# Kernel optimization log

Measured on AMD Instinct MI355X. Metric: run time of the kernel, lower is better.

The kernel has to match this reference:

```python
import jax, jax.numpy as jnp
import numpy as np

N_NODES = 50000
N_EDGES = 800000
NEG_SLOPE = 0.2  # PyG GATConv default


def _gat_layer(x, src, dst, n, W, a_src, a_dst, b, concat):
    """One GATConv layer (PyG semantics, eval mode so attention dropout is off).

    x: [N, F_in], src/dst: [E'] (self loops included), W: [F_in, H*C],
    a_src/a_dst: [H, C], b: [H*C] if concat else [C].
    """
    H, C = a_src.shape
    h = (x @ W).reshape(n, H, C)                      # [N, H, C]
    al_s = jnp.sum(h * a_src, axis=-1)                # [N, H]
    al_d = jnp.sum(h * a_dst, axis=-1)                # [N, H]
    e = jax.nn.leaky_relu(al_s[src] + al_d[dst], NEG_SLOPE)  # [E', H]
    # numerically stable softmax over incoming edges of each dst node
    m = jax.lax.stop_gradient(jax.ops.segment_max(e, dst, num_segments=n))
    m = jnp.where(jnp.isfinite(m), m, 0.0)
    ex = jnp.exp(e - m[dst])                          # [E', H]
    denom = jax.ops.segment_sum(ex, dst, num_segments=n)     # [N, H]
    alpha = ex / denom[dst]                           # safe: self loops => denom > 0
    out = jax.ops.segment_sum(alpha[:, :, None] * h[src], dst, num_segments=n)  # [N,H,C]
    out = out.reshape(n, H * C) if concat else out.mean(axis=1)
    return out + b


def setup_inputs() -> dict:
    key = jax.random.key(0)
    ks = jax.random.split(key, 8)
    in_dim, hid, heads, out_dim = 256, 32, 8, 16
    x = jax.random.normal(ks[0], (N_NODES, in_dim), dtype=jnp.float32)
    edge_index = jax.random.randint(ks[1], (2, N_EDGES), 0, N_NODES, dtype=jnp.int64)
    s1 = 1.0 / np.sqrt(in_dim)
    s2 = 1.0 / np.sqrt(heads * hid)
    return {
        "x": x,
        "edge_index": edge_index,
        "W1": jax.random.normal(ks[2], (in_dim, heads * hid), dtype=jnp.float32) * s1,
        "a_src1": jax.random.normal(ks[3], (heads, hid), dtype=jnp.float32) * s2,
        "a_dst1": jax.random.normal(ks[4], (heads, hid), dtype=jnp.float32) * s2,
        "b1": jnp.zeros((heads * hid,), dtype=jnp.float32),
        "W2": jax.random.normal(ks[5], (heads * hid, out_dim), dtype=jnp.float32) * s2,
        "a_src2": jax.random.normal(ks[6], (1, out_dim), dtype=jnp.float32) * 0.25,
        "a_dst2": jax.random.normal(ks[7], (1, out_dim), dtype=jnp.float32) * 0.25,
        "b2": jnp.zeros((out_dim,), dtype=jnp.float32),
    }


def reference(x, edge_index, W1, a_src1, a_dst1, b1, W2, a_src2, a_dst2, b2):
    n = x.shape[0]
    loops = jnp.arange(n, dtype=edge_index.dtype)
    src = jnp.concatenate([edge_index[0], loops])  # add_self_loops (PyG default)
    dst = jnp.concatenate([edge_index[1], loops])
    h = jax.nn.relu(_gat_layer(x, src, dst, n, W1, a_src1, a_dst1, b1, concat=True))
    # F.dropout(p=0.5, training=False) -> identity in eval mode
    h = _gat_layer(h, src, dst, n, W2, a_src2, a_dst2, b2, concat=False)
    return jax.nn.log_softmax(h, axis=1)
```

## Files before the change

### kernel.cpp

```cpp
#include <hip/hip_runtime.h>
#include <hip/hip_bf16.h>


#define LRELU(x) ((x) > 0.f ? (x) : 0.2f * (x))

typedef __attribute__((ext_vector_type(8))) short short8;
typedef __attribute__((ext_vector_type(8))) unsigned short ushort8;
typedef __attribute__((ext_vector_type(4))) float f32x4;

__device__ inline unsigned short f2b(float f) {
    __hip_bfloat16 h = __float2bfloat16(f);
    return *reinterpret_cast<unsigned short*>(&h);
}
__device__ inline float b2f(unsigned short u) {
    __hip_bfloat16 h;
    *reinterpret_cast<unsigned short*>(&h) = u;
    return __bfloat162float(h);
}


__global__ __launch_bounds__(256) void k_prep(const int* __restrict__ dst, int* deg, int E,
                                              const float* __restrict__ W1,
                                              unsigned short* __restrict__ W1t,
                                              const float* __restrict__ W2,
                                              unsigned short* __restrict__ W2t,
                                              const float* __restrict__ x,
                                              unsigned short* __restrict__ xb,
                                              int NX, int HB) {
    int b = blockIdx.x, t = threadIdx.x;
    if (b < HB) {
        int i = b * 256 + t;
        if (i < E) atomicAdd(&deg[dst[i]], 1);
    } else if (b < HB + 256) {
        int k = b - HB;
        W1t[t * 256 + k] = f2b(W1[k * 256 + t]);
    } else if (b < HB + 256 + 16) {
        int nn = b - HB - 256;
        W2t[nn * 256 + t] = f2b(W2[t * 16 + nn]);
    } else {
        int i = ((b - HB - 272) * 256 + t) * 8;
        if (i < NX) {
            const float4* sp = (const float4*)(x + i);
            float4 f0 = sp[0], f1 = sp[1];
            ushort8 o;
            o[0] = f2b(f0.x); o[1] = f2b(f0.y); o[2] = f2b(f0.z); o[3] = f2b(f0.w);
            o[4] = f2b(f1.x); o[5] = f2b(f1.y); o[6] = f2b(f1.z); o[7] = f2b(f1.w);
            *(ushort8*)(xb + i) = o;
        }
    }
}


__global__ __launch_bounds__(256) void k_scanA(const int* __restrict__ deg,
                                               int* __restrict__ tmp,
                                               int* __restrict__ blocksum, int n) {
    __shared__ int sc[256];
    int b = blockIdx.x, t = threadIdx.x;
    int i = b * 256 + t;
    int v = (i < n) ? deg[i] + 1 : 0;
    sc[t] = v;
    __syncthreads();
    for (int off = 1; off < 256; off <<= 1) {
        int x = 0;
        if (t >= off) x = sc[t - off];
        __syncthreads();
        sc[t] += x;
        __syncthreads();
    }
    if (i < n) tmp[i] = sc[t] - v;
    if (t == 255) blocksum[b] = sc[255];
}


__global__ __launch_bounds__(256) void k_scanC(const int* __restrict__ tmp,
                                               const int* __restrict__ blocksum,
                                               int* __restrict__ offs,
                                               int* __restrict__ cursor,
                                               int n, int P, int nb) {
    __shared__ int sc[256];
    __shared__ int base;
    int b = blockIdx.x, t = threadIdx.x;
    int v = (t < nb) ? blocksum[t] : 0;
    sc[t] = v;
    __syncthreads();
    for (int off = 1; off < 256; off <<= 1) {
        int x = 0;
        if (t >= off) x = sc[t - off];
        __syncthreads();
        sc[t] += x;
        __syncthreads();
    }
    if (t == 0) base = (b == 0) ? 0 : sc[b - 1];
    __syncthreads();
    int i = b * 256 + t;
    if (i < n) {
        int o = tmp[i] + base;
        offs[i] = o;
        cursor[i] = o;
    }
    if (b == 0 && t == 0) offs[n] = P;
}


__global__ __launch_bounds__(256) void k_g1sc(const unsigned short* __restrict__ Ab,
                                              const unsigned short* __restrict__ Wt,
                                              unsigned short* __restrict__ h1b,
                                              const float* __restrict__ asrc,
                                              const float* __restrict__ adst,
                                              float* __restrict__ als,
                                              float* __restrict__ ald, int M, int GB,
                                              const int* __restrict__ src,
                                              const int* __restrict__ dstv,
                                              int* cursor, int* __restrict__ csr, int E) {
    __shared__ unsigned short As[128][40];
    __shared__ unsigned short Bs[128][40];
    int t = threadIdx.x;
    int b = blockIdx.x;
    if (b >= GB) {
        int i = (b - GB) * 256 + t;
        int s, d;
        if (i < E) {
            s = src[i];
            d = dstv[i];
        } else if (i < E + M) {
            s = i - E;
            d = s;
        } else {
            return;
        }
        int p = atomicAdd(&cursor[d], 1);
        csr[p] = s;
        return;
    }
    int r0 = (b >> 1) * 128, c0 = (b & 1) * 128;
    int srow = t >> 1, shalf = t & 1;
    int lane = t & 63, w = t >> 6;
    int lane15 = lane & 15, quad = lane >> 4;
    int rbw = (w & 1) * 64, cbw = (w >> 1) * 64;

    f32x4 acc[4][4];
#pragma unroll
    for (int i = 0; i < 4; i++)
#pragma unroll
        for (int j = 0; j < 4; j++) acc[i][j] = (f32x4)0.f;

    for (int k0 = 0; k0 < 256; k0 += 32) {
        {
            int row = r0 + srow;
            ushort8 p0, p1;
            if (row < M) {
                const ushort8* ap = (const ushort8*)&Ab[(size_t)row * 256 + k0 + shalf * 16];
                p0 = ap[0];
                p1 = ap[1];
            } else {
                p0 = (ushort8)0; p1 = (ushort8)0;
            }
            *(ushort8*)&As[srow][shalf * 16] = p0;
            *(ushort8*)&As[srow][shalf * 16 + 8] = p1;
            const ushort8* bp = (const ushort8*)&Wt[(size_t)(c0 + srow) * 256 + k0 + shalf * 16];
            *(ushort8*)&Bs[srow][shalf * 16] = bp[0];
            *(ushort8*)&Bs[srow][shalf * 16 + 8] = bp[1];
        }
        __syncthreads();
        short8 af[4], bf[4];
#pragma unroll
        for (int i = 0; i < 4; i++)
            af[i] = *(const short8*)&As[rbw + i * 16 + lane15][quad * 8];
#pragma unroll
        for (int j = 0; j < 4; j++)
            bf[j] = *(const short8*)&Bs[cbw + j * 16 + lane15][quad * 8];
#pragma unroll
        for (int i = 0; i < 4; i++)
#pragma unroll
            for (int j = 0; j < 4; j++)
                acc[i][j] = __builtin_amdgcn_mfma_f32_16x16x32_bf16(af[i], bf[j], acc[i][j], 0, 0, 0);
        __syncthreads();
    }

    float asv[4], adv[4];
#pragma unroll
    for (int j = 0; j < 4; j++) {
        asv[j] = asrc[c0 + cbw + j * 16 + lane15];
        adv[j] = adst[c0 + cbw + j * 16 + lane15];
    }
    int hb = (c0 + cbw) >> 5;
#pragma unroll
    for (int i = 0; i < 4; i++) {
        int rowb = r0 + rbw + i * 16 + quad * 4;
#pragma unroll
        for (int j = 0; j < 4; j++) {
            int col = c0 + cbw + j * 16 + lane15;
#pragma unroll
            for (int r = 0; r < 4; r++) {
                int row = rowb + r;
                if (row < M) h1b[(size_t)row * 256 + col] = f2b(acc[i][j][r]);
            }
        }
#pragma unroll
        for (int m = 0; m < 2; m++) {
#pragma unroll
            for (int r = 0; r < 4; r++) {
                float ps = acc[i][2 * m][r] * asv[2 * m] + acc[i][2 * m + 1][r] * asv[2 * m + 1];
                float pd = acc[i][2 * m][r] * adv[2 * m] + acc[i][2 * m + 1][r] * adv[2 * m + 1];
#pragma unroll
                for (int off = 1; off < 16; off <<= 1) {
                    ps += __shfl_xor(ps, off, 16);
                    pd += __shfl_xor(pd, off, 16);
                }
                int row = rowb + r;
                if (lane15 == 0 && row < M) {
                    als[(size_t)row * 8 + hb + m] = ps;
                    ald[(size_t)row * 8 + hb + m] = pd;
                }
            }
        }
    }
}


__global__ __launch_bounds__(128) void k_agg1(const int* __restrict__ csr,
                                              const int* __restrict__ offs,
                                              const float* __restrict__ als,
                                              const float* __restrict__ aldg,
                                              const unsigned short* __restrict__ h1b,
                                              const float* __restrict__ b1,
                                              unsigned short* __restrict__ x2b) {
    int v = blockIdx.x;
    int t = threadIdx.x;
    int start = offs[v];
    int deg = offs[v + 1] - start;
    __shared__ float aldv[8];
    __shared__ int su[32];
    __shared__ float ws[8 * 33];
    if (t < 8) aldv[t] = aldg[v * 8 + t];
    __syncthreads();
    int h = t >> 4;
    const unsigned int* __restrict__ hbase = (const unsigned int*)h1b;
    float a0 = 0.f, a1 = 0.f, wsum = 0.f;
    for (int base = 0; base < deg; base += 32) {
        int cnt = min(32, deg - base);
        int cnt4 = (cnt + 3) & ~3;
        if (base) __syncthreads();
        if (t < cnt4) {
            if (t < cnt) {
                int u = csr[start + base + t];
                su[t] = u;
                const float4* ap = (const float4*)(als + (size_t)u * 8);
                float4 x0 = ap[0], x1 = ap[1];
                ws[0 * 33 + t] = __expf(LRELU(x0.x + aldv[0]));
                ws[1 * 33 + t] = __expf(LRELU(x0.y + aldv[1]));
                ws[2 * 33 + t] = __expf(LRELU(x0.z + aldv[2]));
                ws[3 * 33 + t] = __expf(LRELU(x0.w + aldv[3]));
                ws[4 * 33 + t] = __expf(LRELU(x1.x + aldv[4]));
                ws[5 * 33 + t] = __expf(LRELU(x1.y + aldv[5]));
                ws[6 * 33 + t] = __expf(LRELU(x1.z + aldv[6]));
                ws[7 * 33 + t] = __expf(LRELU(x1.w + aldv[7]));
            } else {
                su[t] = v;
#pragma unroll
                for (int k = 0; k < 8; k++) ws[k * 33 + t] = 0.f;
            }
        }
        __syncthreads();
        for (int e = 0; e < cnt4; e += 4) {
            int u0 = su[e + 0], u1 = su[e + 1], u2 = su[e + 2], u3 = su[e + 3];
            float w0 = ws[h * 33 + e + 0];
            float w1 = ws[h * 33 + e + 1];
            float w2 = ws[h * 33 + e + 2];
            float w3 = ws[h * 33 + e + 3];
            unsigned int pk0 = hbase[u0 * 128 + t];
            unsigned int pk1 = hbase[u1 * 128 + t];
            unsigned int pk2 = hbase[u2 * 128 + t];
            unsigned int pk3 = hbase[u3 * 128 + t];
            a0 += w0 * __uint_as_float(pk0 << 16);
            a1 += w0 * __uint_as_float(pk0 & 0xffff0000u);
            a0 += w1 * __uint_as_float(pk1 << 16);
            a1 += w1 * __uint_as_float(pk1 & 0xffff0000u);
            a0 += w2 * __uint_as_float(pk2 << 16);
            a1 += w2 * __uint_as_float(pk2 & 0xffff0000u);
            a0 += w3 * __uint_as_float(pk3 << 16);
            a1 += w3 * __uint_as_float(pk3 & 0xffff0000u);
            wsum += (w0 + w1) + (w2 + w3);
        }
    }
    const float2* b1v = (const float2*)b1;
    float2 bb = b1v[t];
    float inv = 1.0f / wsum;
    float o0 = a0 * inv + bb.x;
    float o1 = a1 * inv + bb.y;
    o0 = o0 > 0.f ? o0 : 0.f;
    o1 = o1 > 0.f ? o1 : 0.f;
    unsigned int opk = (unsigned int)f2b(o0) | ((unsigned int)f2b(o1) << 16);
    ((unsigned int*)(x2b + (size_t)v * 256))[t] = opk;
}


__global__ __launch_bounds__(256) void k_gemm2(const unsigned short* __restrict__ Xb,
                                               const unsigned short* __restrict__ W2t,
                                               const float* __restrict__ asrc,
                                               const float* __restrict__ adst,
                                               unsigned short* __restrict__ h2b,
                                               float* __restrict__ als,
                                               float* __restrict__ ald, int n) {
    int t = threadIdx.x;
    int lane = t & 63, w = t >> 6;
    int lane15 = lane & 15, quad = lane >> 4;
    int row0 = blockIdx.x * 64 + w * 16;
    f32x4 acc = (f32x4)0.f;
#pragma unroll
    for (int k0 = 0; k0 < 256; k0 += 32) {
        short8 a = *(const short8*)&Xb[(size_t)(row0 + lane15) * 256 + k0 + quad * 8];
        short8 b = *(const short8*)&W2t[lane15 * 256 + k0 + quad * 8];
        acc = __builtin_amdgcn_mfma_f32_16x16x32_bf16(a, b, acc, 0, 0, 0);
    }
    float asv = asrc[lane15], adv = adst[lane15];
#pragma unroll
    for (int r = 0; r < 4; r++) {
        int row = row0 + quad * 4 + r;
        float hv = acc[r];
        float ps = hv * asv, pd = hv * adv;
#pragma unroll
        for (int off = 1; off < 16; off <<= 1) {
            ps += __shfl_xor(ps, off, 16);
            pd += __shfl_xor(pd, off, 16);
        }
        if (row < n) {
            h2b[(size_t)row * 16 + lane15] = f2b(hv);
            if (lane15 == 0) {
                als[row] = ps;
                ald[row] = pd;
            }
        }
    }
}


__global__ __launch_bounds__(256) void k_agg2(const int* __restrict__ csr,
                                              const int* __restrict__ offs,
                                              const float* __restrict__ als,
                                              const float* __restrict__ aldg,
                                              const unsigned short* __restrict__ h2b,
                                              const float* __restrict__ b2,
                                              float* __restrict__ out, int n) {
    int v = blockIdx.x * 4 + (threadIdx.x >> 6);
    if (v >= n) return;
    int lane = threadIdx.x & 63;
    int start = offs[v];
    int deg = offs[v + 1] - start;
    float aldv = aldg[v];
    int c = lane & 15, q = lane >> 4;
    float acc = 0.f, wsum = 0.f;
    for (int e = q; e < deg; e += 4) {
        int u = csr[start + e];
        float x = als[u] + aldv;
        float wv = __expf(LRELU(x));
        acc += wv * b2f(h2b[(size_t)u * 16 + c]);
        wsum += wv;
    }
    acc += __shfl_xor(acc, 32, 64);
    acc += __shfl_xor(acc, 16, 64);
    wsum += __shfl_xor(wsum, 32, 64);
    wsum += __shfl_xor(wsum, 16, 64);
    float o = acc / wsum + b2[c];
    float mx = o;
#pragma unroll
    for (int off = 8; off; off >>= 1) mx = fmaxf(mx, __shfl_xor(mx, off, 16));
    float s = __expf(o - mx);
#pragma unroll
    for (int off = 8; off; off >>= 1) s += __shfl_xor(s, off, 16);
    float res = o - mx - __logf(s);
    if (q == 0) out[(size_t)v * 16 + c] = res;
}


extern "C" void kernel_launch(void* const* d_in, const int* in_sizes, int n_in,
                              void* d_out, int out_size, void* d_ws, size_t ws_size,
                              hipStream_t stream) {
    const float* x = (const float*)d_in[0];
    const int* ei = (const int*)d_in[1];
    const float* W1 = (const float*)d_in[2];
    const float* asrc1 = (const float*)d_in[3];
    const float* adst1 = (const float*)d_in[4];
    const float* b1 = (const float*)d_in[5];
    const float* W2 = (const float*)d_in[6];
    const float* asrc2 = (const float*)d_in[7];
    const float* adst2 = (const float*)d_in[8];
    const float* b2 = (const float*)d_in[9];
    float* out = (float*)d_out;

    int n = in_sizes[0] / 256;
    int E = in_sizes[1] / 2;
    int P = E + n;
    const int* src = ei;
    const int* dst = ei + E;
    int NB = (n + 255) / 256;
    int HB = (E + 255) / 256;
    int NX = n * 256;
    int XB = (NX + 2047) / 2048;
    int GB = ((n + 127) / 128) * 2;
    int SB = (P + 255) / 256;

    char* p = (char*)d_ws;
    auto alloc = [&](size_t bytes) {
        void* r = (void*)p;
        p += (bytes + 255) & ~(size_t)255;
        return r;
    };
    unsigned short* h1b = (unsigned short*)alloc((size_t)n * 256 * 2);
    unsigned short* x2b = (unsigned short*)alloc((size_t)n * 256 * 2);
    unsigned short* xb = (unsigned short*)alloc((size_t)n * 256 * 2);
    unsigned short* W1t = (unsigned short*)alloc((size_t)256 * 256 * 2);
    unsigned short* W2t = (unsigned short*)alloc((size_t)16 * 256 * 2);
    float* als1 = (float*)alloc((size_t)n * 8 * 4);
    float* ald1 = (float*)alloc((size_t)n * 8 * 4);
    unsigned short* h2b = (unsigned short*)alloc((size_t)n * 16 * 2);
    float* als2 = (float*)alloc((size_t)n * 4);
    float* ald2 = (float*)alloc((size_t)n * 4);
    int* deg = (int*)alloc((size_t)n * 4);
    int* offs = (int*)alloc((size_t)(n + 1) * 4);
    int* cursor = (int*)alloc((size_t)n * 4);
    int* stmp = (int*)alloc((size_t)n * 4);
    int* blocksum = (int*)alloc((size_t)NB * 4);
    int* csr = (int*)alloc((size_t)P * 4);

    hipMemsetAsync(deg, 0, (size_t)n * 4, stream);
    k_prep<<<HB + 272 + XB, 256, 0, stream>>>(dst, deg, E, W1, W1t, W2, W2t, x, xb, NX, HB);
    k_scanA<<<NB, 256, 0, stream>>>(deg, stmp, blocksum, n);
    k_scanC<<<NB, 256, 0, stream>>>(stmp, blocksum, offs, cursor, n, P, NB);

    k_g1sc<<<GB + SB, 256, 0, stream>>>(xb, W1t, h1b, asrc1, adst1, als1, ald1, n, GB,
                                        src, dst, cursor, csr, E);
    k_agg1<<<n, 128, 0, stream>>>(csr, offs, als1, ald1, h1b, b1, x2b);

    k_gemm2<<<(n + 63) / 64, 256, 0, stream>>>(x2b, W2t, asrc2, adst2, h2b, als2, ald2, n);
    k_agg2<<<(n + 3) / 4, 256, 0, stream>>>(csr, offs, als2, ald2, h2b, b2, out, n);
}
```

Measured before the change: 341.2 us.

## Merge CSR build and weight/input conversion into one cooperative kernel

```diff
diff --git a/kernel.cpp b/kernel.cpp
--- a/kernel.cpp
+++ b/kernel.cpp
@@ -1,6 +1,9 @@
 #include <hip/hip_runtime.h>
 #include <hip/hip_bf16.h>
-
+#include <hip/hip_cooperative_groups.h>
+
+
+namespace cg = cooperative_groups;
 
 #define LRELU(x) ((x) > 0.f ? (x) : 0.2f * (x))
 
@@ -19,120 +22,112 @@
 }
 
 
-__global__ __launch_bounds__(256) void k_prep(const int* __restrict__ dst, int* deg, int E,
-                                              const float* __restrict__ W1,
-                                              unsigned short* __restrict__ W1t,
-                                              const float* __restrict__ W2,
-                                              unsigned short* __restrict__ W2t,
-                                              const float* __restrict__ x,
-                                              unsigned short* __restrict__ xb,
-                                              int NX, int HB) {
-    int b = blockIdx.x, t = threadIdx.x;
-    if (b < HB) {
-        int i = b * 256 + t;
-        if (i < E) atomicAdd(&deg[dst[i]], 1);
-    } else if (b < HB + 256) {
-        int k = b - HB;
-        W1t[t * 256 + k] = f2b(W1[k * 256 + t]);
-    } else if (b < HB + 256 + 16) {
-        int nn = b - HB - 256;
-        W2t[nn * 256 + t] = f2b(W2[t * 16 + nn]);
-    } else {
-        int i = ((b - HB - 272) * 256 + t) * 8;
-        if (i < NX) {
-            const float4* sp = (const float4*)(x + i);
-            float4 f0 = sp[0], f1 = sp[1];
-            ushort8 o;
-            o[0] = f2b(f0.x); o[1] = f2b(f0.y); o[2] = f2b(f0.z); o[3] = f2b(f0.w);
-            o[4] = f2b(f1.x); o[5] = f2b(f1.y); o[6] = f2b(f1.z); o[7] = f2b(f1.w);
-            *(ushort8*)(xb + i) = o;
-        }
-    }
-}
-
-
-__global__ __launch_bounds__(256) void k_scanA(const int* __restrict__ deg,
-                                               int* __restrict__ tmp,
-                                               int* __restrict__ blocksum, int n) {
-    __shared__ int sc[256];
-    int b = blockIdx.x, t = threadIdx.x;
-    int i = b * 256 + t;
-    int v = (i < n) ? deg[i] + 1 : 0;
-    sc[t] = v;
-    __syncthreads();
-    for (int off = 1; off < 256; off <<= 1) {
-        int x = 0;
-        if (t >= off) x = sc[t - off];
-        __syncthreads();
-        sc[t] += x;
-        __syncthreads();
-    }
-    if (i < n) tmp[i] = sc[t] - v;
-    if (t == 255) blocksum[b] = sc[255];
-}
-
-
-__global__ __launch_bounds__(256) void k_scanC(const int* __restrict__ tmp,
-                                               const int* __restrict__ blocksum,
-                                               int* __restrict__ offs,
-                                               int* __restrict__ cursor,
-                                               int n, int P, int nb) {
+__global__ __launch_bounds__(256) void k_csr(const int* __restrict__ src,
+                                             const int* __restrict__ dst,
+                                             int* deg, int* tmp, int* blocksum,
+                                             int* offs, int* cursor, int* __restrict__ csr,
+                                             const float* __restrict__ W1,
+                                             unsigned short* __restrict__ W1t,
+                                             const float* __restrict__ W2,
+                                             unsigned short* __restrict__ W2t,
+                                             const float* __restrict__ x,
+                                             unsigned short* __restrict__ xb,
+                                             int n, int E, int P, int NB, int NX) {
+    cg::grid_group grid = cg::this_grid();
     __shared__ int sc[256];
     __shared__ int base;
     int b = blockIdx.x, t = threadIdx.x;
-    int v = (t < nb) ? blocksum[t] : 0;
-    sc[t] = v;
-    __syncthreads();
-    for (int off = 1; off < 256; off <<= 1) {
-        int x = 0;
-        if (t >= off) x = sc[t - off];
-        __syncthreads();
-        sc[t] += x;
-        __syncthreads();
-    }
-    if (t == 0) base = (b == 0) ? 0 : sc[b - 1];
-    __syncthreads();
-    int i = b * 256 + t;
-    if (i < n) {
-        int o = tmp[i] + base;
-        offs[i] = o;
-        cursor[i] = o;
-    }
-    if (b == 0 && t == 0) offs[n] = P;
-}
-
-
-__global__ __launch_bounds__(256) void k_g1sc(const unsigned short* __restrict__ Ab,
-                                              const unsigned short* __restrict__ Wt,
-                                              unsigned short* __restrict__ h1b,
-                                              const float* __restrict__ asrc,
-                                              const float* __restrict__ adst,
-                                              float* __restrict__ als,
-                                              float* __restrict__ ald, int M, int GB,
-                                              const int* __restrict__ src,
-                                              const int* __restrict__ dstv,
-                                              int* cursor, int* __restrict__ csr, int E) {
+    int gid = b * 256 + t;
+    int gsz = gridDim.x * 256;
+
+    for (int i = gid; i < n; i += gsz) deg[i] = 0;
+    for (int i = gid; i < 65536; i += gsz) {
+        int k = i >> 8, nn = i & 255;
+        W1t[nn * 256 + k] = f2b(W1[k * 256 + nn]);
+    }
+    for (int i = gid; i < 4096; i += gsz) {
+        int nn = i >> 8, k = i & 255;
+        W2t[nn * 256 + k] = f2b(W2[k * 16 + nn]);
+    }
+    for (int i = gid * 8; i < NX; i += gsz * 8) {
+        const float4* sp = (const float4*)(x + i);
+        float4 f0 = sp[0], f1 = sp[1];
+        ushort8 o;
+        o[0] = f2b(f0.x); o[1] = f2b(f0.y); o[2] = f2b(f0.z); o[3] = f2b(f0.w);
+        o[4] = f2b(f1.x); o[5] = f2b(f1.y); o[6] = f2b(f1.z); o[7] = f2b(f1.w);
+        *(ushort8*)(xb + i) = o;
+    }
+    grid.sync();
+
+    for (int i = gid; i < E; i += gsz) atomicAdd(&deg[dst[i]], 1);
+    grid.sync();
+
+    if (b < NB) {
+        int i = b * 256 + t;
+        int v = (i < n) ? deg[i] + 1 : 0;
+        sc[t] = v;
+        __syncthreads();
+        for (int off = 1; off < 256; off <<= 1) {
+            int xx = 0;
+            if (t >= off) xx = sc[t - off];
+            __syncthreads();
+            sc[t] += xx;
+            __syncthreads();
+        }
+        if (i < n) tmp[i] = sc[t] - v;
+        if (t == 255) blocksum[b] = sc[255];
+    }
+    grid.sync();
+
+    if (b < NB) {
+        int v = (t < NB) ? blocksum[t] : 0;
+        sc[t] = v;
+        __syncthreads();
+        for (int off = 1; off < 256; off <<= 1) {
+            int xx = 0;
+            if (t >= off) xx = sc[t - off];
+            __syncthreads();
+            sc[t] += xx;
+            __syncthreads();
+        }
+        if (t == 0) base = (b == 0) ? 0 : sc[b - 1];
+        __syncthreads();
+        int i = b * 256 + t;
+        if (i < n) {
+            int o = tmp[i] + base;
+            offs[i] = o;
+            cursor[i] = o;
+        }
+        if (b == 0 && t == 0) offs[n] = P;
+    }
+    grid.sync();
+
+    for (int i = gid; i < P; i += gsz) {
+        int s, d;
+        if (i < E) {
+            s = src[i];
+            d = dst[i];
+        } else {
+            s = i - E;
+            d = s;
+        }
+        int p = atomicAdd(&cursor[d], 1);
+        csr[p] = s;
+    }
+}
+
+
+__global__ __launch_bounds__(256) void k_gemm1(const unsigned short* __restrict__ Ab,
+                                               const unsigned short* __restrict__ Wt,
+                                               unsigned short* __restrict__ h1b,
+                                               const float* __restrict__ asrc,
+                                               const float* __restrict__ adst,
+                                               float* __restrict__ als,
+                                               float* __restrict__ ald, int M) {
     __shared__ unsigned short As[128][40];
     __shared__ unsigned short Bs[128][40];
     int t = threadIdx.x;
-    int b = blockIdx.x;
-    if (b >= GB) {
-        int i = (b - GB) * 256 + t;
-        int s, d;
-        if (i < E) {
-            s = src[i];
-            d = dstv[i];
-        } else if (i < E + M) {
-            s = i - E;
-            d = s;
-        } else {
-            return;
-        }
-        int p = atomicAdd(&cursor[d], 1);
-        csr[p] = s;
-        return;
-    }
-    int r0 = (b >> 1) * 128, c0 = (b & 1) * 128;
+    int r0 = blockIdx.x * 128, c0 = blockIdx.y * 128;
     int srow = t >> 1, shalf = t & 1;
     int lane = t & 63, w = t >> 6;
     int lane15 = lane & 15, quad = lane >> 4;
@@ -394,11 +389,7 @@
     const int* src = ei;
     const int* dst = ei + E;
     int NB = (n + 255) / 256;
-    int HB = (E + 255) / 256;
     int NX = n * 256;
-    int XB = (NX + 2047) / 2048;
-    int GB = ((n + 127) / 128) * 2;
-    int SB = (P + 255) / 256;
 
     char* p = (char*)d_ws;
     auto alloc = [&](size_t bytes) {
@@ -423,13 +414,20 @@
     int* blocksum = (int*)alloc((size_t)NB * 4);
     int* csr = (int*)alloc((size_t)P * 4);
 
-    hipMemsetAsync(deg, 0, (size_t)n * 4, stream);
-    k_prep<<<HB + 272 + XB, 256, 0, stream>>>(dst, deg, E, W1, W1t, W2, W2t, x, xb, NX, HB);
-    k_scanA<<<NB, 256, 0, stream>>>(deg, stmp, blocksum, n);
-    k_scanC<<<NB, 256, 0, stream>>>(stmp, blocksum, offs, cursor, n, P, NB);
-
-    k_g1sc<<<GB + SB, 256, 0, stream>>>(xb, W1t, h1b, asrc1, adst1, als1, ald1, n, GB,
-                                        src, dst, cursor, csr, E);
+    {
+        void* kargs[] = {
+            (void*)&src, (void*)&dst, (void*)&deg, (void*)&stmp, (void*)&blocksum,
+            (void*)&offs, (void*)&cursor, (void*)&csr,
+            (void*)&W1, (void*)&W1t, (void*)&W2, (void*)&W2t,
+            (void*)&x, (void*)&xb,
+            (void*)&n, (void*)&E, (void*)&P, (void*)&NB, (void*)&NX,
+        };
+        hipLaunchCooperativeKernel((const void*)k_csr, dim3(1024), dim3(256),
+                                   kargs, 0, stream);
+    }
+
+    k_gemm1<<<dim3((n + 127) / 128, 2), 256, 0, stream>>>(xb, W1t, h1b, asrc1, adst1,
+                                                          als1, ald1, n);
     k_agg1<<<n, 128, 0, stream>>>(csr, offs, als1, ald1, h1b, b1, x2b);
 
     k_gemm2<<<(n + 63) / 64, 256, 0, stream>>>(x2b, W2t, asrc2, adst2, h2b, als2, ald2, n);
```

New measurement: 811.3 us. 138% more time.
